# Kernel optimization log

Hardware: AMD Instinct MI355X
Metric: run time of the kernel (lower is better)

The kernel has to match this reference:

```python
import jax, jax.numpy as jnp
import numpy as np

D_MODEL = 1024
N_HEADS = 16
D_HEAD = D_MODEL // N_HEADS


def setup_inputs() -> dict:
    key = jax.random.key(0)
    k1, k2, k3 = jax.random.split(key, 3)
    B, T = 4, 2048
    x = jax.random.normal(k1, (B, T, D_MODEL), dtype=jnp.float32)
    # torch nn.Linear weights: (out_features, in_features), scaled init
    w_qkv = jax.random.normal(k2, (3 * D_MODEL, D_MODEL), dtype=jnp.float32) / np.sqrt(D_MODEL)
    w_out = jax.random.normal(k3, (D_MODEL, D_MODEL), dtype=jnp.float32) / np.sqrt(D_MODEL)
    return {"x": x, "w_qkv": w_qkv, "w_out": w_out}


def reference(x, w_qkv, w_out):
    B, T, _ = x.shape
    qkv = jnp.einsum('btd,ed->bte', x, w_qkv)  # (B,T,3*d_model)
    q, k, v = jnp.split(qkv, 3, axis=-1)
    # (B,T,H,dh) -> (B,H,T,dh)
    def heads(t):
        return t.reshape(B, T, N_HEADS, D_HEAD).transpose(0, 2, 1, 3)
    q, k, v = heads(q), heads(k), heads(v)
    scores = jnp.einsum('bhqd,bhkd->bhqk', q, k) / jnp.sqrt(jnp.float32(D_HEAD))
    causal = jnp.tril(jnp.ones((T, T), dtype=bool))  # True = keep
    scores = jnp.where(causal, scores, -jnp.inf)
    weights = jax.nn.softmax(scores, axis=-1)
    out = jnp.einsum('bhqk,bhkd->bhqd', weights, v)
    out = out.transpose(0, 2, 1, 3).reshape(B, T, D_MODEL)
    return jnp.einsum('btd,ed->bte', out, w_out)
```

## Files before the change

kernel.cpp:

```cpp
#include <hip/hip_runtime.h>

typedef __attribute__((ext_vector_type(8))) short short8;
typedef __attribute__((ext_vector_type(4))) float f32x4;
typedef __attribute__((ext_vector_type(4))) unsigned short us4;
typedef unsigned short u16;

#define MFMA16(a, b, c) __builtin_amdgcn_mfma_f32_16x16x32_bf16(a, b, c, 0, 0, 0)

static __device__ __forceinline__ u16 f2bf(float f) {
  union { float f; unsigned u; } v; v.f = f;
  unsigned r = v.u + 0x7fffu + ((v.u >> 16) & 1u);
  return (u16)(r >> 16);
}

static __device__ __forceinline__ unsigned cvtpk(float lo, float hi) {
  unsigned r;
  asm("v_cvt_pk_bf16_f32 %0, %1, %2" : "=v"(r) : "v"(lo), "v"(hi));
  return r;
}

static __device__ __forceinline__ void gl_lds16(const u16* g, u16* l) {
  __builtin_amdgcn_global_load_lds((const __attribute__((address_space(1))) void*)g,
                                   (__attribute__((address_space(3))) void*)l,
                                   16, 0, 0);
}

__global__ __launch_bounds__(256)
void cvt_bf16(const float* __restrict__ src, u16* __restrict__ dst, int n8)
{
  int i = blockIdx.x * 256 + threadIdx.x;
  const int stride = gridDim.x * 256;
  for (; i < n8; i += stride) {
    f32x4 a = ((const f32x4*)src)[2 * i];
    f32x4 b = ((const f32x4*)src)[2 * i + 1];
    short8 o;
    o[0] = (short)f2bf(a[0]); o[1] = (short)f2bf(a[1]);
    o[2] = (short)f2bf(a[2]); o[3] = (short)f2bf(a[3]);
    o[4] = (short)f2bf(b[0]); o[5] = (short)f2bf(b[1]);
    o[6] = (short)f2bf(b[2]); o[7] = (short)f2bf(b[3]);
    ((short8*)dst)[i] = o;
  }
}

template<int MODE>
__global__ __launch_bounds__(256)
void gemm_bt(const u16* __restrict__ A, const u16* __restrict__ B,
             u16* __restrict__ outp, float* __restrict__ outf)
{
  __shared__ u16 Ash[128 * 32];
  __shared__ u16 Bsh[128 * 32];
  const int tid = threadIdx.x;
  const int lane = tid & 63;
  const int l15 = lane & 15, g = lane >> 4;
  const int w = tid >> 6;
  const int wr = w >> 1, wc = w & 1;

  const int bid = blockIdx.x;
  const int xcd = bid & 7, idx = bid >> 3;
  const int cx = xcd & 3, cy = xcd >> 2;
  int mt, nt;
  if (MODE == 1) {
    mt = cx * 16 + (idx & 15);
    nt = cy * 12 + (idx >> 4);
  } else {
    mt = cx * 16 + (idx & 15);
    nt = cy * 4 + (idx >> 4);
  }
  const long m0 = (long)mt * 128;
  const long n0 = (long)nt * 128;

  f32x4 acc[4][4] = {};

  const int c0 = tid, c1 = tid + 256;
  const long arow0 = m0 + (c0 >> 2), arow1 = m0 + (c1 >> 2);
  const u16* pa0;
  const u16* pa1;
  if (MODE == 2) {
    int b0 = (int)(arow0 >> 11), t0 = (int)(arow0 & 2047);
    int b1 = (int)(arow1 >> 11), t1 = (int)(arow1 & 2047);
    pa0 = A + (size_t)(b0 * 16) * 131072u + (size_t)t0 * 64u + (c0 & 3) * 8;
    pa1 = A + (size_t)(b1 * 16) * 131072u + (size_t)t1 * 64u + (c1 & 3) * 8;
  } else {
    pa0 = A + arow0 * 1024 + (c0 & 3) * 8;
    pa1 = A + arow1 * 1024 + (c1 & 3) * 8;
  }
  const u16* pb0 = B + (n0 + (c0 >> 2)) * 1024 + (c0 & 3) * 8;
  const u16* pb1 = B + (n0 + (c1 >> 2)) * 1024 + (c1 & 3) * 8;
  u16* la0 = Ash + c0 * 8;
  u16* la1 = Ash + c1 * 8;
  u16* lb0 = Bsh + c0 * 8;
  u16* lb1 = Bsh + c1 * 8;

  const u16* afp[4];
  const u16* bfp[4];
  #pragma unroll
  for (int mi = 0; mi < 4; ++mi)
    afp[mi] = &Ash[(wr * 64 + mi * 16 + l15) * 32 + g * 8];
  #pragma unroll
  for (int ni = 0; ni < 4; ++ni)
    bfp[ni] = &Bsh[(wc * 64 + ni * 16 + l15) * 32 + g * 8];

  for (int k0 = 0; k0 < 1024; k0 += 32) {
    __syncthreads();
    gl_lds16(pa0, la0); gl_lds16(pa1, la1);
    gl_lds16(pb0, lb0); gl_lds16(pb1, lb1);
    if (MODE == 2) {
      long d = (k0 & 32) ? (131072 - 32) : 32;
      pa0 += d; pa1 += d;
    } else {
      pa0 += 32; pa1 += 32;
    }
    pb0 += 32; pb1 += 32;
    __syncthreads();

    short8 af[4], bf[4];
    #pragma unroll
    for (int mi = 0; mi < 4; ++mi) af[mi] = *(const short8*)afp[mi];
    #pragma unroll
    for (int ni = 0; ni < 4; ++ni) bf[ni] = *(const short8*)bfp[ni];
    #pragma unroll
    for (int mi = 0; mi < 4; ++mi)
      #pragma unroll
      for (int ni = 0; ni < 4; ++ni)
        acc[mi][ni] = MFMA16(af[mi], bf[ni], acc[mi][ni]);
  }

  if (MODE == 2) {
    #pragma unroll
    for (int mi = 0; mi < 4; ++mi) {
      long m = m0 + wr * 64 + mi * 16 + g * 4;
      #pragma unroll
      for (int ni = 0; ni < 4; ++ni) {
        int n = (int)n0 + wc * 64 + ni * 16 + l15;
        #pragma unroll
        for (int r = 0; r < 4; ++r)
          outf[(m + r) * 1024 + n] = acc[mi][ni][r];
      }
    }
  } else {
    #pragma unroll
    for (int mi = 0; mi < 4; ++mi) {
      long m = m0 + wr * 64 + mi * 16 + g * 4;
      int b = (int)(m >> 11);
      int t = (int)(m & 2047);
      #pragma unroll
      for (int ni = 0; ni < 4; ++ni) {
        int e = (int)n0 + wc * 64 + ni * 16 + l15;
        int sel = e >> 10;
        int ee = e & 1023;
        int h = ee >> 6, dh = ee & 63;
        size_t bh131k = (size_t)(b * 16 + h) * 131072u;
        if (sel < 2) {
          float sc = (sel == 0) ? 0.125f : 1.0f;
          size_t base = (size_t)sel * 8388608u + bh131k + (size_t)t * 64u + dh;
          #pragma unroll
          for (int r = 0; r < 4; ++r)
            outp[base + (size_t)r * 64u] = f2bf(acc[mi][ni][r] * sc);
        } else {
          size_t base = 16777216u + bh131k + (size_t)dh * 2048u + (size_t)t;
          us4 v;
          #pragma unroll
          for (int r = 0; r < 4; ++r) v[r] = f2bf(acc[mi][ni][r]);
          *(us4*)&outp[base] = v;
        }
      }
    }
  }
}

__global__ __launch_bounds__(512, 4)
void attn(const u16* __restrict__ Q, const u16* __restrict__ K,
          const u16* __restrict__ VT, u16* __restrict__ O)
{
  __shared__ u16 Ksh[2][64 * 64];
  __shared__ u16 Vsh[2][64 * 64];
  __shared__ u16 Psh[8][16 * 64];

  const int tid = threadIdx.x;
  const int lane = tid & 63;
  const int l15 = lane & 15, g = lane >> 4;
  const int w = tid >> 6;
  const int bid = blockIdx.x;
  const int qi = 7 - (bid >> 6);
  const int bh = bid & 63;
  const int q0 = qi * 256;
  const int qb = q0 + w * 32;
  const int nt = qi * 4 + 4;

  const u16* Qp = Q + (size_t)bh * 131072u;
  const u16* Kp = K + (size_t)bh * 131072u;
  const u16* Vp = VT + (size_t)bh * 131072u;

  short8 qf[2][2];
  #pragma unroll
  for (int mi = 0; mi < 2; ++mi)
    #pragma unroll
    for (int kc = 0; kc < 2; ++kc)
      qf[mi][kc] = *(const short8*)&Qp[(qb + mi * 16 + l15) * 64 + kc * 32 + g * 8];

  f32x4 oacc[2][4] = {};
  float mrun[2] = {-1e30f, -1e30f};
  float lrun[2] = {0.f, 0.f};

  const int rA = tid >> 3, uA = ((tid & 7) ^ (rA & 7)) * 8;

#define STAGE(kv0s, b) do {                                            \
    gl_lds16(Kp + ((kv0s) + rA) * 64 + uA, Ksh[b] + tid * 8);          \
    gl_lds16(Vp + (size_t)rA * 2048u + (kv0s) + uA, Vsh[b] + tid * 8); \
  } while (0)

  STAGE(0, 0);
  int cur = 0;

  for (int ti = 0; ti < nt; ++ti) {
    const int kv0 = ti * 64;
    if (ti + 1 < nt) {
      STAGE(kv0 + 64, cur ^ 1);
      asm volatile("s_waitcnt vmcnt(2)" ::: "memory");
    } else {
      asm volatile("s_waitcnt vmcnt(0)" ::: "memory");
    }
    __builtin_amdgcn_s_barrier();
    __builtin_amdgcn_sched_barrier(0);

    if (kv0 <= qb + 31) {
      const u16* Kb = Ksh[cur];
      const u16* Vb = Vsh[cur];

      f32x4 s[2][4] = {};
      #pragma unroll
      for (int kc = 0; kc < 2; ++kc)
        #pragma unroll
        for (int ni = 0; ni < 4; ++ni) {
          int row = ni * 16 + l15;
          short8 kb = *(const short8*)&Kb[row * 64 + (((kc * 4 + g) ^ (row & 7)) << 3)];
          #pragma unroll
          for (int mi = 0; mi < 2; ++mi)
            s[mi][ni] = MFMA16(kb, qf[mi][kc], s[mi][ni]);
        }

      if (kv0 + 63 > qb) {
        #pragma unroll
        for (int mi = 0; mi < 2; ++mi) {
          int qv = qb + mi * 16 + l15;
          #pragma unroll
          for (int ni = 0; ni < 4; ++ni)
            #pragma unroll
            for (int r = 0; r < 4; ++r)
              if (kv0 + ni * 16 + g * 4 + r > qv)
                s[mi][ni][r] = -1e30f;
        }
      }

      #pragma unroll
      for (int mi = 0; mi < 2; ++mi) {
        float mx0 = fmaxf(fmaxf(s[mi][0][0], s[mi][0][1]),
                          fmaxf(s[mi][0][2], s[mi][0][3]));
        float mx1 = fmaxf(fmaxf(s[mi][1][0], s[mi][1][1]),
                          fmaxf(s[mi][1][2], s[mi][1][3]));
        float mx2 = fmaxf(fmaxf(s[mi][2][0], s[mi][2][1]),
                          fmaxf(s[mi][2][2], s[mi][2][3]));
        float mx3 = fmaxf(fmaxf(s[mi][3][0], s[mi][3][1]),
                          fmaxf(s[mi][3][2], s[mi][3][3]));
        float mx = fmaxf(fmaxf(mx0, mx1), fmaxf(mx2, mx3));
        mx = fmaxf(mx, __shfl_xor(mx, 16));
        mx = fmaxf(mx, __shfl_xor(mx, 32));
        if (!__all(mx - mrun[mi] <= 8.0f)) {
          float mn = fmaxf(mrun[mi], mx);
          float sc = __expf(mrun[mi] - mn);
          mrun[mi] = mn;
          lrun[mi] *= sc;
          #pragma unroll
          for (int nj = 0; nj < 4; ++nj) {
            oacc[mi][nj][0] *= sc;
            oacc[mi][nj][1] *= sc;
            oacc[mi][nj][2] *= sc;
            oacc[mi][nj][3] *= sc;
          }
        }
        float mn = mrun[mi];
        float rs = 0.f;
        #pragma unroll
        for (int ni = 0; ni < 4; ++ni)
          #pragma unroll
          for (int r = 0; r < 4; ++r) {
            float p = __expf(s[mi][ni][r] - mn);
            s[mi][ni][r] = p;
            rs += p;
          }
        rs += __shfl_xor(rs, 16);
        rs += __shfl_xor(rs, 32);
        lrun[mi] += rs;
      }

      u16* Pw = &Psh[w][0];
      short8 pb[2][2];
      #pragma unroll
      for (int mi = 0; mi < 2; ++mi) {
        #pragma unroll
        for (int ni = 0; ni < 4; ++ni) {
          int col = ni * 16 + g * 4;
          uint2 pv;
          pv.x = cvtpk(s[mi][ni][0], s[mi][ni][1]);
          pv.y = cvtpk(s[mi][ni][2], s[mi][ni][3]);
          *(uint2*)&Pw[l15 * 64 + (col ^ ((l15 & 7) << 3))] = pv;
        }
        #pragma unroll
        for (int kc = 0; kc < 2; ++kc)
          pb[mi][kc] = *(const short8*)&Pw[l15 * 64 + (((kc * 4 + g) ^ (l15 & 7)) << 3)];
      }

      #pragma unroll
      for (int kc = 0; kc < 2; ++kc)
        #pragma unroll
        for (int nj = 0; nj < 4; ++nj) {
          int vrow = nj * 16 + l15;
          short8 vb = *(const short8*)&Vb[vrow * 64 + (((kc * 4 + g) ^ (vrow & 7)) << 3)];
          #pragma unroll
          for (int mi = 0; mi < 2; ++mi)
            oacc[mi][nj] = MFMA16(vb, pb[mi][kc], oacc[mi][nj]);
        }
    }

    __builtin_amdgcn_sched_barrier(0);
    __builtin_amdgcn_s_barrier();
    cur ^= 1;
  }
#undef STAGE

  #pragma unroll
  for (int mi = 0; mi < 2; ++mi) {
    float inv = 1.0f / lrun[mi];
    int t = qb + mi * 16 + l15;
    size_t base = (size_t)bh * 131072u + (size_t)t * 64u;
    #pragma unroll
    for (int nj = 0; nj < 4; ++nj) {
      uint2 o;
      o.x = cvtpk(oacc[mi][nj][0] * inv, oacc[mi][nj][1] * inv);
      o.y = cvtpk(oacc[mi][nj][2] * inv, oacc[mi][nj][3] * inv);
      *(uint2*)&O[base + nj * 16 + g * 4] = o;
    }
  }
}

extern "C" void kernel_launch(void* const* d_in, const int* in_sizes, int n_in,
                              void* d_out, int out_size, void* d_ws, size_t ws_size,
                              hipStream_t stream)
{
  (void)in_sizes; (void)n_in; (void)out_size; (void)ws_size;
  const float* x    = (const float*)d_in[0];
  const float* wqkv = (const float*)d_in[1];
  const float* wout = (const float*)d_in[2];
  u16* ws  = (u16*)d_ws;
  u16* Qw   = ws;
  u16* Kw   = ws + 8388608;
  u16* VTw  = ws + 16777216;
  u16* wqb  = ws + 25165824;
  u16* wob  = ws + 28311552;
  u16* xb   = (u16*)d_out;
  float* y  = (float*)d_out;

  hipLaunchKernelGGL(cvt_bf16, dim3(2048), dim3(256), 0, stream, x,    xb,  1048576);
  hipLaunchKernelGGL(cvt_bf16, dim3(1536), dim3(256), 0, stream, wqkv, wqb, 393216);
  hipLaunchKernelGGL(cvt_bf16, dim3(512),  dim3(256), 0, stream, wout, wob, 131072);
  hipLaunchKernelGGL((gemm_bt<1>), dim3(1536), dim3(256), 0, stream, xb, wqb, ws, (float*)nullptr);
  hipLaunchKernelGGL(attn,         dim3(512),  dim3(512), 0, stream, Qw, Kw, VTw, Qw);
  hipLaunchKernelGGL((gemm_bt<2>), dim3(512),  dim3(256), 0, stream, Qw, wob, (u16*)nullptr, y);
}
```

Measured before the change: 191.4 us.

## Replace QKV GEMM with 256x256-tile double-buffered swizzled-LDS kernel

The QKV projection moves from a 128x128-tile, 256-thread GEMM with two syncthreads per k-step to a new 256x256-tile, 512-thread kernel. The new kernel double-buffers LDS with async global-to-LDS loads and partial vmcnt waits. It also XOR-swizzles the LDS layout to avoid bank conflicts and raises wave priority around the MFMA block. The aim is more data reuse per tile and overlap of loads with compute, at the cost of higher register and LDS use and only 384 blocks for the grid.

```diff
diff --git a/kernel.cpp b/kernel.cpp
--- a/kernel.cpp
+++ b/kernel.cpp
@@ -42,10 +42,131 @@
   }
 }
 
-template<int MODE>
+__global__ __launch_bounds__(512, 2)
+void gemm256_qkv(const u16* __restrict__ A, const u16* __restrict__ B,
+                 u16* __restrict__ outp)
+{
+  __shared__ u16 Ash[2][8192];
+  __shared__ u16 Bsh[2][8192];
+
+  const int tid = threadIdx.x;
+  const int lane = tid & 63;
+  const int l15 = lane & 15, g = lane >> 4;
+  const int w = tid >> 6;
+  const int wr = w >> 2, wc = w & 3;
+
+  const int bid = blockIdx.x;
+  const int xcd = bid & 7, idx = bid >> 3;
+  const int cx = xcd & 3, cy = xcd >> 2;
+  const int mt = cx * 8 + (idx & 7);
+  const int nt = cy * 6 + (idx >> 3);
+  const long m0 = (long)mt * 256;
+  const long n0 = (long)nt * 256;
+
+  f32x4 acc[8][4] = {};
+
+  const int c0 = tid, c1 = tid + 512;
+  const int li0 = c0 >> 3, lp0 = (c0 & 7) ^ (li0 & 7);
+  const int li1 = c1 >> 3, lp1 = (c1 & 7) ^ (li1 & 7);
+  const int r0 = 2 * li0 + (lp0 >> 2), e0 = (lp0 & 3) * 8;
+  const int r1 = 2 * li1 + (lp1 >> 2), e1 = (lp1 & 3) * 8;
+  const u16* pa0 = A + (m0 + r0) * 1024 + e0;
+  const u16* pa1 = A + (m0 + r1) * 1024 + e1;
+  const u16* pb0 = B + (n0 + r0) * 1024 + e0;
+  const u16* pb1 = B + (n0 + r1) * 1024 + e1;
+
+  int aoff[8], boff[4];
+  #pragma unroll
+  for (int mi = 0; mi < 8; ++mi) {
+    int row = wr * 128 + mi * 16 + l15;
+    int line = row >> 1;
+    int p = (((row & 1) << 2) | g) ^ (line & 7);
+    aoff[mi] = line * 64 + p * 8;
+  }
+  #pragma unroll
+  for (int nj = 0; nj < 4; ++nj) {
+    int row = wc * 64 + nj * 16 + l15;
+    int line = row >> 1;
+    int p = (((row & 1) << 2) | g) ^ (line & 7);
+    boff[nj] = line * 64 + p * 8;
+  }
+
+#define STAGE(kt, b) do {                              \
+    gl_lds16(pa0 + (kt) * 32, &Ash[b][c0 * 8]);        \
+    gl_lds16(pa1 + (kt) * 32, &Ash[b][c1 * 8]);        \
+    gl_lds16(pb0 + (kt) * 32, &Bsh[b][c0 * 8]);        \
+    gl_lds16(pb1 + (kt) * 32, &Bsh[b][c1 * 8]);        \
+  } while (0)
+
+  STAGE(0, 0);
+  STAGE(1, 1);
+  int cur = 0;
+
+  for (int kt = 0; kt < 32; ++kt) {
+    if (kt < 31) {
+      asm volatile("s_waitcnt vmcnt(4)" ::: "memory");
+    } else {
+      asm volatile("s_waitcnt vmcnt(0)" ::: "memory");
+    }
+    __builtin_amdgcn_sched_barrier(0);
+    __builtin_amdgcn_s_barrier();
+    __builtin_amdgcn_sched_barrier(0);
+
+    const u16* Ab = &Ash[cur][0];
+    const u16* Bb = &Bsh[cur][0];
+    short8 bf[4], af[8];
+    #pragma unroll
+    for (int nj = 0; nj < 4; ++nj) bf[nj] = *(const short8*)&Bb[boff[nj]];
+    #pragma unroll
+    for (int mi = 0; mi < 8; ++mi) af[mi] = *(const short8*)&Ab[aoff[mi]];
+    __builtin_amdgcn_s_setprio(1);
+    #pragma unroll
+    for (int mi = 0; mi < 8; ++mi)
+      #pragma unroll
+      for (int nj = 0; nj < 4; ++nj)
+        acc[mi][nj] = MFMA16(af[mi], bf[nj], acc[mi][nj]);
+    __builtin_amdgcn_s_setprio(0);
+
+    __builtin_amdgcn_sched_barrier(0);
+    __builtin_amdgcn_s_barrier();
+    __builtin_amdgcn_sched_barrier(0);
+    if (kt < 30) STAGE(kt + 2, cur);
+    cur ^= 1;
+  }
+#undef STAGE
+
+  #pragma unroll
+  for (int mi = 0; mi < 8; ++mi) {
+    long m = m0 + wr * 128 + mi * 16 + g * 4;
+    int b = (int)(m >> 11);
+    int t = (int)(m & 2047);
+    #pragma unroll
+    for (int nj = 0; nj < 4; ++nj) {
+      int e = (int)n0 + wc * 64 + nj * 16 + l15;
+      int sel = e >> 10;
+      int ee = e & 1023;
+      int h = ee >> 6, dh = ee & 63;
+      size_t bh131k = (size_t)(b * 16 + h) * 131072u;
+      if (sel < 2) {
+        float sc = (sel == 0) ? 0.125f : 1.0f;
+        size_t base = (size_t)sel * 8388608u + bh131k + (size_t)t * 64u + dh;
+        #pragma unroll
+        for (int r = 0; r < 4; ++r)
+          outp[base + (size_t)r * 64u] = f2bf(acc[mi][nj][r] * sc);
+      } else {
+        size_t base = 16777216u + bh131k + (size_t)dh * 2048u + (size_t)t;
+        us4 v;
+        #pragma unroll
+        for (int r = 0; r < 4; ++r) v[r] = f2bf(acc[mi][nj][r]);
+        *(us4*)&outp[base] = v;
+      }
+    }
+  }
+}
+
 __global__ __launch_bounds__(256)
-void gemm_bt(const u16* __restrict__ A, const u16* __restrict__ B,
-             u16* __restrict__ outp, float* __restrict__ outf)
+void gemm_out(const u16* __restrict__ A, const u16* __restrict__ B,
+              float* __restrict__ outf)
 {
   __shared__ u16 Ash[128 * 32];
   __shared__ u16 Bsh[128 * 32];
@@ -58,14 +179,8 @@
   const int bid = blockIdx.x;
   const int xcd = bid & 7, idx = bid >> 3;
   const int cx = xcd & 3, cy = xcd >> 2;
-  int mt, nt;
-  if (MODE == 1) {
-    mt = cx * 16 + (idx & 15);
-    nt = cy * 12 + (idx >> 4);
-  } else {
-    mt = cx * 16 + (idx & 15);
-    nt = cy * 4 + (idx >> 4);
-  }
+  const int mt = cx * 16 + (idx & 15);
+  const int nt = cy * 4 + (idx >> 4);
   const long m0 = (long)mt * 128;
   const long n0 = (long)nt * 128;
 
@@ -73,17 +188,10 @@
 
   const int c0 = tid, c1 = tid + 256;
   const long arow0 = m0 + (c0 >> 2), arow1 = m0 + (c1 >> 2);
-  const u16* pa0;
-  const u16* pa1;
-  if (MODE == 2) {
-    int b0 = (int)(arow0 >> 11), t0 = (int)(arow0 & 2047);
-    int b1 = (int)(arow1 >> 11), t1 = (int)(arow1 & 2047);
-    pa0 = A + (size_t)(b0 * 16) * 131072u + (size_t)t0 * 64u + (c0 & 3) * 8;
-    pa1 = A + (size_t)(b1 * 16) * 131072u + (size_t)t1 * 64u + (c1 & 3) * 8;
-  } else {
-    pa0 = A + arow0 * 1024 + (c0 & 3) * 8;
-    pa1 = A + arow1 * 1024 + (c1 & 3) * 8;
-  }
+  int b0 = (int)(arow0 >> 11), t0 = (int)(arow0 & 2047);
+  int b1 = (int)(arow1 >> 11), t1 = (int)(arow1 & 2047);
+  const u16* pa0 = A + (size_t)(b0 * 16) * 131072u + (size_t)t0 * 64u + (c0 & 3) * 8;
+  const u16* pa1 = A + (size_t)(b1 * 16) * 131072u + (size_t)t1 * 64u + (c1 & 3) * 8;
   const u16* pb0 = B + (n0 + (c0 >> 2)) * 1024 + (c0 & 3) * 8;
   const u16* pb1 = B + (n0 + (c1 >> 2)) * 1024 + (c1 & 3) * 8;
   u16* la0 = Ash + c0 * 8;
@@ -104,12 +212,8 @@
     __syncthreads();
     gl_lds16(pa0, la0); gl_lds16(pa1, la1);
     gl_lds16(pb0, lb0); gl_lds16(pb1, lb1);
-    if (MODE == 2) {
-      long d = (k0 & 32) ? (131072 - 32) : 32;
-      pa0 += d; pa1 += d;
-    } else {
-      pa0 += 32; pa1 += 32;
-    }
+    long d = (k0 & 32) ? (131072 - 32) : 32;
+    pa0 += d; pa1 += d;
     pb0 += 32; pb1 += 32;
     __syncthreads();
 
@@ -125,45 +229,15 @@
         acc[mi][ni] = MFMA16(af[mi], bf[ni], acc[mi][ni]);
   }
 
-  if (MODE == 2) {
-    #pragma unroll
-    for (int mi = 0; mi < 4; ++mi) {
-      long m = m0 + wr * 64 + mi * 16 + g * 4;
-      #pragma unroll
-      for (int ni = 0; ni < 4; ++ni) {
-        int n = (int)n0 + wc * 64 + ni * 16 + l15;
-        #pragma unroll
-        for (int r = 0; r < 4; ++r)
-          outf[(m + r) * 1024 + n] = acc[mi][ni][r];
-      }
-    }
-  } else {
-    #pragma unroll
-    for (int mi = 0; mi < 4; ++mi) {
-      long m = m0 + wr * 64 + mi * 16 + g * 4;
-      int b = (int)(m >> 11);
-      int t = (int)(m & 2047);
-      #pragma unroll
-      for (int ni = 0; ni < 4; ++ni) {
-        int e = (int)n0 + wc * 64 + ni * 16 + l15;
-        int sel = e >> 10;
-        int ee = e & 1023;
-        int h = ee >> 6, dh = ee & 63;
-        size_t bh131k = (size_t)(b * 16 + h) * 131072u;
-        if (sel < 2) {
-          float sc = (sel == 0) ? 0.125f : 1.0f;
-          size_t base = (size_t)sel * 8388608u + bh131k + (size_t)t * 64u + dh;
-          #pragma unroll
-          for (int r = 0; r < 4; ++r)
-            outp[base + (size_t)r * 64u] = f2bf(acc[mi][ni][r] * sc);
-        } else {
-          size_t base = 16777216u + bh131k + (size_t)dh * 2048u + (size_t)t;
-          us4 v;
-          #pragma unroll
-          for (int r = 0; r < 4; ++r) v[r] = f2bf(acc[mi][ni][r]);
-          *(us4*)&outp[base] = v;
-        }
-      }
+  #pragma unroll
+  for (int mi = 0; mi < 4; ++mi) {
+    long m = m0 + wr * 64 + mi * 16 + g * 4;
+    #pragma unroll
+    for (int ni = 0; ni < 4; ++ni) {
+      int n = (int)n0 + wc * 64 + ni * 16 + l15;
+      #pragma unroll
+      for (int r = 0; r < 4; ++r)
+        outf[(m + r) * 1024 + n] = acc[mi][ni][r];
     }
   }
 }
@@ -363,7 +437,7 @@
   hipLaunchKernelGGL(cvt_bf16, dim3(2048), dim3(256), 0, stream, x,    xb,  1048576);
   hipLaunchKernelGGL(cvt_bf16, dim3(1536), dim3(256), 0, stream, wqkv, wqb, 393216);
   hipLaunchKernelGGL(cvt_bf16, dim3(512),  dim3(256), 0, stream, wout, wob, 131072);
-  hipLaunchKernelGGL((gemm_bt<1>), dim3(1536), dim3(256), 0, stream, xb, wqb, ws, (float*)nullptr);
-  hipLaunchKernelGGL(attn,         dim3(512),  dim3(512), 0, stream, Qw, Kw, VTw, Qw);
-  hipLaunchKernelGGL((gemm_bt<2>), dim3(512),  dim3(256), 0, stream, Qw, wob, (u16*)nullptr, y);
-}
+  hipLaunchKernelGGL(gemm256_qkv, dim3(384), dim3(512), 0, stream, xb, wqb, ws);
+  hipLaunchKernelGGL(attn,        dim3(512), dim3(512), 0, stream, Qw, Kw, VTw, Qw);
+  hipLaunchKernelGGL(gemm_out,    dim3(512), dim3(256), 0, stream, Qw, wob, y);
+}
```

After: 198.0 us. 3.5% more time.
